# Kernel tuning notes

Hardware: AMD Instinct MI355X
Metric: run time of the kernel (lower is better)

Reference implementation:

```python
import jax, jax.numpy as jnp
import numpy as np

EPS = 1e-12


def _l2norm(x, axis):
    return x / jnp.maximum(jnp.linalg.norm(x, axis=axis, keepdims=True), EPS)


def _wn_weight(v, g):
    # weight norm over input axis (kernel_size=1): W = g * v / ||v||
    return g * v / jnp.maximum(jnp.linalg.norm(v, axis=0, keepdims=True), EPS)


def setup_inputs() -> dict:
    key = jax.random.key(0)
    ks = jax.random.split(key, 8)
    B, T, D = 16, 4096, 512
    N, K, d = 9, 1024, 8
    return {
        "z": jax.random.normal(ks[0], (B, T, D), dtype=jnp.float32),
        "in_v": jax.random.normal(ks[1], (N, D, d), dtype=jnp.float32) * 0.05,
        "in_g": jax.random.uniform(ks[2], (N, d), dtype=jnp.float32) + 0.5,
        "in_b": jax.random.normal(ks[3], (N, d), dtype=jnp.float32) * 0.01,
        "out_v": jax.random.normal(ks[4], (N, d, D), dtype=jnp.float32) * 0.05,
        "out_g": jax.random.uniform(ks[5], (N, D), dtype=jnp.float32) + 0.5,
        "out_b": jax.random.normal(ks[6], (N, D), dtype=jnp.float32) * 0.01,
        "codebooks": jax.random.normal(ks[7], (N, K, d), dtype=jnp.float32),
    }


def reference(z, in_v, in_g, in_b, out_v, out_g, out_b, codebooks):
    # Eval-mode ResidualVectorQuantize: n_quantizers = n_codebooks, mask all True.
    n_codebooks = codebooks.shape[0]
    residual = z
    z_q = jnp.zeros_like(z)
    commitment_loss = jnp.zeros((), z.dtype)
    codebook_loss = jnp.zeros((), z.dtype)
    codes, latents = [], []
    for i in range(n_codebooks):
        # in_proj (weight-normalized 1x1 conv == linear): [B,T,D] -> [B,T,d]
        W_in = _wn_weight(in_v[i], in_g[i])
        z_e = jnp.einsum("btd,dc->btc", residual, W_in) + in_b[i]
        # decode_latents: l2-normalize, pairwise sq-dist, nearest neighbor
        cb = codebooks[i]                      # [K, d] raw codebook
        enc_n = _l2norm(z_e, axis=-1)          # [B, T, d]
        cb_n = _l2norm(cb, axis=-1)            # [K, d]
        dist = (jnp.sum(enc_n * enc_n, -1, keepdims=True)
                - 2.0 * jnp.einsum("btc,kc->btk", enc_n, cb_n)
                + jnp.sum(cb_n * cb_n, -1))    # [B, T, K]
        indices = jnp.argmax(-dist, axis=-1)   # [B, T]
        z_q_i = cb[indices]                    # gather from raw codebook [B,T,d]
        # per-batch losses (mean over T, d)
        commit_i = jnp.mean((z_e - jax.lax.stop_gradient(z_q_i)) ** 2, axis=(1, 2))
        cbloss_i = jnp.mean((z_q_i - jax.lax.stop_gradient(z_e)) ** 2, axis=(1, 2))
        # straight-through estimator
        z_q_st = z_e + jax.lax.stop_gradient(z_q_i - z_e)
        # out_proj: [B,T,d] -> [B,T,D]
        W_out = _wn_weight(out_v[i], out_g[i])
        z_q_proj = jnp.einsum("btc,cd->btd", z_q_st, W_out) + out_b[i]
        z_q = z_q + z_q_proj
        residual = residual - z_q_proj
        commitment_loss = commitment_loss + commit_i.mean()
        codebook_loss = codebook_loss + cbloss_i.mean()
        codes.append(indices)
        latents.append(z_e)
    codes = jnp.stack(codes, axis=2)           # [B, T, N]
    latents = jnp.concatenate(latents, axis=2) # [B, T, N*d]
    return z_q, codes, latents, commitment_loss, codebook_loss
```

## Files before the change

kernel.cpp:

```cpp
#include <hip/hip_runtime.h>
#include <math.h>

#define ROWS   65536

#define WS_WPAD 0
#define WS_WOUT 49152
#define WS_CBT  86016
#define WS_SC   159744
#define WS_M    168960
#define WS_CACC 174144
#define WS_SOB  174216
#define WS_LOSS 174728

#define OUT_CODES 33554432
#define OUT_LAT   34144256
#define OUT_CLOSS 38862848
#define OUT_CBLOSS 38862849

__device__ __forceinline__ int pcol(int cc){ return (cc/9)*12 + (cc%9); }

__global__ __launch_bounds__(256) void prep1(const float* __restrict__ in_v,
    const float* __restrict__ in_g, const float* __restrict__ out_v,
    const float* __restrict__ out_g, const float* __restrict__ out_b,
    const float* __restrict__ cb, float* __restrict__ ws)
{
    int t = blockIdx.x*256 + threadIdx.x;
    if (t < 9216) {
        int i = t >> 10, k = t & 1023;
        const float* p = cb + (i*1024 + k)*8;
        float v[8]; float ssq = 0.f;
        #pragma unroll
        for (int c=0;c<8;c++){ v[c]=p[c]; ssq = fmaf(v[c],v[c],ssq); }
        float den = fmaxf(sqrtf(ssq), 1e-12f);
        float sc = 0.f;
        #pragma unroll
        for (int c=0;c<8;c++){ float cn = v[c]/den; ws[WS_CBT + (i*8+c)*1024 + k] = cn; sc = fmaf(cn,cn,sc); }
        ws[WS_SC + i*1024 + k] = sc;
    } else if (t < 13824) {
        int r = t - 9216; int j = r >> 9, tt = r & 511;
        float v[8]; float ssq = 0.f;
        #pragma unroll
        for (int a=0;a<8;a++){ v[a]=out_v[(j*8+a)*512+tt]; ssq=fmaf(v[a],v[a],ssq); }
        float den = fmaxf(sqrtf(ssq), 1e-12f);
        float g = out_g[j*512+tt];
        #pragma unroll
        for (int a=0;a<8;a++) ws[WS_WOUT + (j*8+a)*512 + tt] = g*v[a]/den;
    } else if (t < 18432) {
        int r = t - 13824;
        int w = r >> 6, l = r & 63;
        int i = w >> 3, c = w & 7;
        float v[8]; float ssq = 0.f;
        #pragma unroll
        for (int u=0;u<8;u++){ v[u] = in_v[(i*512 + l*8+u)*8 + c]; ssq = fmaf(v[u],v[u],ssq); }
        #pragma unroll
        for (int off=1; off<64; off<<=1) ssq += __shfl_xor(ssq, off, 64);
        float den = fmaxf(sqrtf(ssq), 1e-12f);
        float g = in_g[i*8+c];
        int pc = pcol(i*8+c);
        #pragma unroll
        for (int u=0;u<8;u++) ws[WS_WPAD + (l*8+u)*96 + pc] = g*v[u]/den;
    } else if (t < 18944) {
        int tt = t - 18432;
        float s = 0.f;
        for (int j=0;j<9;j++) s += out_b[j*512+tt];
        ws[WS_SOB + tt] = s;
    } else if (t == 18944) {
        *(double*)&ws[WS_LOSS] = 0.0;
    }
}

__global__ __launch_bounds__(256) void prep2(const float* __restrict__ out_b,
                                             float* __restrict__ ws)
{
    int g = blockIdx.x*256 + threadIdx.x;
    if (g < 41472) {
        int oi = g >> 3, part = g & 7;
        int j = oi / 576; int rem = oi % 576; int i = rem >> 6; int ab = rem & 63;
        int a = ab >> 3, b = ab & 7;
        int pc = pcol(i*8+b);
        const float* wo = ws + WS_WOUT + (j*8+a)*512 + part*64;
        const float* wp = ws + WS_WPAD + (part*64)*96 + pc;
        float s = 0.f;
        #pragma unroll
        for (int u=0; u<16; u++) {
            float4 w4 = *(const float4*)(wo + u*4);
            s = fmaf(w4.x, wp[(u*4+0)*96], s);
            s = fmaf(w4.y, wp[(u*4+1)*96], s);
            s = fmaf(w4.z, wp[(u*4+2)*96], s);
            s = fmaf(w4.w, wp[(u*4+3)*96], s);
        }
        #pragma unroll
        for (int off=1; off<8; off<<=1) s += __shfl_xor(s, off, 64);
        if (part == 0) ws[WS_M + oi] = s;
    } else if (g < 42048) {
        int r = g - 41472;
        int oi = r >> 3, part = r & 7;
        int i = oi >> 3, b = oi & 7;
        int pc = pcol(i*8+b);
        float s = 0.f;
        for (int u=0; u<64; u++) {
            int tt = part*64 + u;
            float bb = 0.f;
            for (int j=0;j<i;j++) bb += out_b[j*512+tt];
            s = fmaf(bb, ws[WS_WPAD + tt*96+pc], s);
        }
        #pragma unroll
        for (int off=1; off<8; off<<=1) s += __shfl_xor(s, off, 64);
        if (part == 0) ws[WS_CACC + oi] = s;
    }
}

__global__ __launch_bounds__(256) void gemm_in(const float* __restrict__ z,
    const float* __restrict__ in_b, const float* __restrict__ ws, float* __restrict__ out)
{
    __shared__ float AsT[32*132];
    __shared__ float Bs[32*96];
    int tid = threadIdx.x;
    int rowbase = blockIdx.x * 128;
    int tr = tid & 31, tc = tid >> 5;
    float acc[4][9];
    #pragma unroll
    for (int r=0;r<4;r++){
        #pragma unroll
        for(int c=0;c<9;c++) acc[r][c]=0.f;
    }
    int kq = tid & 7, rr = tid >> 3;
    for (int kk=0; kk<16; kk++) {
        #pragma unroll
        for (int p=0;p<4;p++){
            int row = rr + p*32;
            float4 a = *(const float4*)(z + (size_t)(rowbase+row)*512 + kk*32 + kq*4);
            AsT[(kq*4+0)*132 + row] = a.x;
            AsT[(kq*4+1)*132 + row] = a.y;
            AsT[(kq*4+2)*132 + row] = a.z;
            AsT[(kq*4+3)*132 + row] = a.w;
        }
        #pragma unroll
        for (int p=0;p<3;p++){
            int idx = p*256 + tid;
            *(float4*)(Bs + idx*4) = *(const float4*)(ws + WS_WPAD + kk*32*96 + idx*4);
        }
        __syncthreads();
        #pragma unroll 4
        for (int k=0;k<32;k++){
            float4 a  = *(const float4*)(AsT + k*132 + tr*4);
            float4 b0 = *(const float4*)(Bs + k*96 + tc*12);
            float4 b1 = *(const float4*)(Bs + k*96 + tc*12 + 4);
            float  b8 = Bs[k*96 + tc*12 + 8];
            float av[4] = {a.x,a.y,a.z,a.w};
            float bv[9] = {b0.x,b0.y,b0.z,b0.w,b1.x,b1.y,b1.z,b1.w,b8};
            #pragma unroll
            for (int r=0;r<4;r++){
                #pragma unroll
                for (int c=0;c<9;c++) acc[r][c] = fmaf(av[r], bv[c], acc[r][c]);
            }
        }
        __syncthreads();
    }
    #pragma unroll
    for (int c=0;c<9;c++){
        int cc = tc*9+c;
        float bias = in_b[cc];
        #pragma unroll
        for (int r=0;r<4;r++){
            int row = rowbase + tr*4 + r;
            out[OUT_LAT + (size_t)row*72 + cc] = acc[r][c] + bias;
        }
    }
}

__global__ __launch_bounds__(512, 4) void step_all(
    const float* __restrict__ cbooks, float* __restrict__ ws, float* __restrict__ out)
{
    __shared__ float lds_cb[8*1056];
    __shared__ float lds_sc[8*132];
    __shared__ float codes_lds[128*13];
    __shared__ float warr[8];

    int tid = threadIdx.x;
    int oct = tid & 7;
    int rowslot = tid >> 3;
    int rowbase = blockIdx.x * 128;
    const int kbase = oct*128;
    const float* cbo = lds_cb + oct*132;
    const float* sco = lds_sc + oct*132;

    float lacc = 0.f;

    for (int i=0; i<9; i++){
        __syncthreads();
        #pragma unroll
        for (int p=0;p<4;p++){
            int s = (p*512 + tid)*4;
            int c = s >> 10; int k = s & 1023; int o = k >> 7; int kk = k & 127;
            float4 v = *(const float4*)(ws + WS_CBT + i*8192 + s);
            *(float4*)(lds_cb + c*1056 + o*132 + kk) = v;
        }
        if (tid < 256){
            int s = tid*4;
            int o = s >> 7; int kk = s & 127;
            float4 v = *(const float4*)(ws + WS_SC + i*1024 + s);
            v.x *= 0.5f; v.y *= 0.5f; v.z *= 0.5f; v.w *= 0.5f;
            *(float4*)(lds_sc + o*132 + kk) = v;
        }
        __syncthreads();

        float zen[2][8];
        #pragma unroll
        for (int r=0;r<2;r++){
            int rib = r*64 + rowslot;
            int row = rowbase + rib;
            float* lat = out + OUT_LAT + (size_t)row*72 + i*8;
            float4 p0 = *(const float4*)(lat);
            float4 p1 = *(const float4*)(lat+4);
            float ze[8] = {p0.x,p0.y,p0.z,p0.w,p1.x,p1.y,p1.z,p1.w};
            #pragma unroll
            for (int b=0;b<8;b++) ze[b] -= ws[WS_CACC + i*8 + b];
            for (int j=0;j<i;j++){
                int kj = (int)codes_lds[rib*13 + j];
                const float* qp = cbooks + (size_t)(j*1024+kj)*8;
                float4 q0 = *(const float4*)(qp);
                float4 q1 = *(const float4*)(qp+4);
                float qa[8] = {q0.x,q0.y,q0.z,q0.w,q1.x,q1.y,q1.z,q1.w};
                const float* M = ws + WS_M + (j*9+i)*64;
                #pragma unroll
                for (int a=0;a<8;a++){
                    #pragma unroll
                    for (int b=0;b<8;b++) ze[b] = fmaf(-qa[a], M[a*8+b], ze[b]);
                }
            }
            float ssq = 0.f;
            #pragma unroll
            for (int c=0;c<8;c++) ssq = fmaf(ze[c],ze[c],ssq);
            float den = fmaxf(sqrtf(ssq), 1e-12f);
            float rden = 1.0f/den;
            if (oct == 0){
                float4 z0 = {ze[0],ze[1],ze[2],ze[3]};
                float4 z1 = {ze[4],ze[5],ze[6],ze[7]};
                *(float4*)(lat)   = z0;
                *(float4*)(lat+4) = z1;
            }
            #pragma unroll
            for (int c=0;c<8;c++) zen[r][c] = ze[c]*rden;
        }

        float bv[2]; int bk[2];
        #pragma unroll
        for (int r=0;r<2;r++){ bv[r] = -3.0e38f; bk[r] = kbase; }
        #pragma unroll 2
        for (int kk=0; kk<128; kk+=4){
            float4 v[8];
            #pragma unroll
            for (int c=0;c<8;c++) v[c] = *(const float4*)(cbo + c*1056 + kk);
            float4 hs = *(const float4*)(sco + kk);
            #pragma unroll
            for (int r=0;r<2;r++){
                float d0=-hs.x, d1=-hs.y, d2=-hs.z, d3=-hs.w;
                #pragma unroll
                for (int c=0;c<8;c++){
                    d0 = fmaf(zen[r][c], v[c].x, d0);
                    d1 = fmaf(zen[r][c], v[c].y, d1);
                    d2 = fmaf(zen[r][c], v[c].z, d2);
                    d3 = fmaf(zen[r][c], v[c].w, d3);
                }
                bool c0 = d0 > bv[r]; bk[r] = c0?(kbase+kk+0):bk[r]; bv[r] = c0?d0:bv[r];
                bool c1 = d1 > bv[r]; bk[r] = c1?(kbase+kk+1):bk[r]; bv[r] = c1?d1:bv[r];
                bool c2 = d2 > bv[r]; bk[r] = c2?(kbase+kk+2):bk[r]; bv[r] = c2?d2:bv[r];
                bool c3 = d3 > bv[r]; bk[r] = c3?(kbase+kk+3):bk[r]; bv[r] = c3?d3:bv[r];
            }
        }

        #pragma unroll
        for (int off=1; off<8; off<<=1){
            #pragma unroll
            for (int r=0;r<2;r++){
                float ov = __shfl_xor(bv[r], off, 64);
                int   ok = __shfl_xor(bk[r], off, 64);
                bool rep = (ov > bv[r]) || (ov == bv[r] && ok < bk[r]);
                bv[r] = rep ? ov : bv[r];
                bk[r] = rep ? ok : bk[r];
            }
        }
        if (oct == 0){
            #pragma unroll
            for (int r=0;r<2;r++){
                int rib = r*64 + rowslot;
                int row = rowbase + rib;
                out[OUT_CODES + (size_t)row*9 + i] = (float)bk[r];
                codes_lds[rib*13 + i] = (float)bk[r];
                const float* lat = out + OUT_LAT + (size_t)row*72 + i*8;
                const float* qp = cbooks + (size_t)(i*1024+bk[r])*8;
                float4 z0 = *(const float4*)(lat);
                float4 z1 = *(const float4*)(lat+4);
                float4 q0 = *(const float4*)(qp);
                float4 q1 = *(const float4*)(qp+4);
                float e0 = z0.x-q0.x, e1 = z0.y-q0.y, e2 = z0.z-q0.z, e3 = z0.w-q0.w;
                float e4 = z1.x-q1.x, e5 = z1.y-q1.y, e6 = z1.z-q1.z, e7 = z1.w-q1.w;
                lacc = fmaf(e0,e0,lacc); lacc = fmaf(e1,e1,lacc);
                lacc = fmaf(e2,e2,lacc); lacc = fmaf(e3,e3,lacc);
                lacc = fmaf(e4,e4,lacc); lacc = fmaf(e5,e5,lacc);
                lacc = fmaf(e6,e6,lacc); lacc = fmaf(e7,e7,lacc);
            }
        }
    }

    #pragma unroll
    for (int off=1; off<64; off<<=1) lacc += __shfl_xor(lacc, off, 64);
    if ((tid & 63)==0) warr[tid>>6] = lacc;
    __syncthreads();
    if (tid==0){
        double bs = 0.0;
        #pragma unroll
        for (int w=0; w<8; w++) bs += (double)warr[w];
        atomicAdd((double*)&ws[WS_LOSS], bs);
    }
}

__global__ __launch_bounds__(256) void gemm_out(const float* __restrict__ cbooks,
    const float* __restrict__ ws, float* __restrict__ out)
{
    __shared__ float QLT[72*140];
    __shared__ float Ws[72*140];
    int tid = threadIdx.x;
    int rowbase = blockIdx.x*128;
    if (tid < 128){
        int row = rowbase + tid;
        int rsw = tid + (tid>>5)*4;
        for (int j=0;j<9;j++){
            int kj = (int)out[OUT_CODES + (size_t)row*9 + j];
            const float* qp = cbooks + (size_t)(j*1024+kj)*8;
            float4 q0 = *(const float4*)qp;
            float4 q1 = *(const float4*)(qp+4);
            QLT[(j*8+0)*140 + rsw] = q0.x;
            QLT[(j*8+1)*140 + rsw] = q0.y;
            QLT[(j*8+2)*140 + rsw] = q0.z;
            QLT[(j*8+3)*140 + rsw] = q0.w;
            QLT[(j*8+4)*140 + rsw] = q1.x;
            QLT[(j*8+5)*140 + rsw] = q1.y;
            QLT[(j*8+6)*140 + rsw] = q1.z;
            QLT[(j*8+7)*140 + rsw] = q1.w;
        }
    }
    int tc = tid & 15, tr = tid >> 4;
    int aoff = tr*8 + (tr>>2)*4;
    int boff = tc*8 + (tc>>2)*4;
    for (int cc=0; cc<4; cc++){
        __syncthreads();
        #pragma unroll
        for (int p=0;p<9;p++){
            int idx = p*256 + tid;
            int jr = idx >> 5; int cq = idx & 31;
            float4 w = *(const float4*)(ws + WS_WOUT + jr*512 + cc*128 + cq*4);
            *(float4*)(Ws + jr*140 + cq*4 + (cq>>3)*4) = w;
        }
        __syncthreads();
        float acc[8][8];
        #pragma unroll
        for (int r=0;r<8;r++){
            #pragma unroll
            for (int c=0;c<8;c++) acc[r][c]=0.f;
        }
        #pragma unroll 2
        for (int k=0;k<72;k++){
            float4 a0 = *(const float4*)(QLT + k*140 + aoff);
            float4 a1 = *(const float4*)(QLT + k*140 + aoff + 4);
            float4 b0 = *(const float4*)(Ws + k*140 + boff);
            float4 b1 = *(const float4*)(Ws + k*140 + boff + 4);
            float av[8] = {a0.x,a0.y,a0.z,a0.w,a1.x,a1.y,a1.z,a1.w};
            float bw[8] = {b0.x,b0.y,b0.z,b0.w,b1.x,b1.y,b1.z,b1.w};
            #pragma unroll
            for (int r=0;r<8;r++){
                #pragma unroll
                for (int c=0;c<8;c++) acc[r][c] = fmaf(av[r], bw[c], acc[r][c]);
            }
        }
        float4 s0 = *(const float4*)(ws + WS_SOB + cc*128 + tc*8);
        float4 s1 = *(const float4*)(ws + WS_SOB + cc*128 + tc*8 + 4);
        #pragma unroll
        for (int r=0;r<8;r++){
            int row = rowbase + tr*8 + r;
            float4 o0 = {acc[r][0]+s0.x, acc[r][1]+s0.y, acc[r][2]+s0.z, acc[r][3]+s0.w};
            float4 o1 = {acc[r][4]+s1.x, acc[r][5]+s1.y, acc[r][6]+s1.z, acc[r][7]+s1.w};
            *(float4*)(out + (size_t)row*512 + cc*128 + tc*8)     = o0;
            *(float4*)(out + (size_t)row*512 + cc*128 + tc*8 + 4) = o1;
        }
    }
    if (blockIdx.x==0 && tid==0){
        double L = *(const double*)(ws + WS_LOSS);
        float lv = (float)(L * (1.0/524288.0));
        out[OUT_CLOSS]  = lv;
        out[OUT_CBLOSS] = lv;
    }
}

extern "C" void kernel_launch(void* const* d_in, const int* in_sizes, int n_in,
                              void* d_out, int out_size, void* d_ws, size_t ws_size,
                              hipStream_t stream) {
    const float* z     = (const float*)d_in[0];
    const float* in_v  = (const float*)d_in[1];
    const float* in_g  = (const float*)d_in[2];
    const float* in_b  = (const float*)d_in[3];
    const float* out_v = (const float*)d_in[4];
    const float* out_g = (const float*)d_in[5];
    const float* out_b = (const float*)d_in[6];
    const float* cb    = (const float*)d_in[7];
    float* out = (float*)d_out;
    float* ws  = (float*)d_ws;

    prep1<<<75, 256, 0, stream>>>(in_v, in_g, out_v, out_g, out_b, cb, ws);
    prep2<<<165, 256, 0, stream>>>(out_b, ws);
    gemm_in<<<512, 256, 0, stream>>>(z, in_b, ws, out);
    step_all<<<512, 512, 0, stream>>>(cb, ws, out);
    gemm_out<<<512, 256, 0, stream>>>(cb, ws, out);
}
```

Measured before the change: 677.2 us.

## Hold codebook slice in registers and reduce argmax across full wavefront

Restructures the nearest-codebook search so each lane keeps 16 codebook entries in registers and sweeps all 32 rows of its wave, with normalized latents shared via LDS. Removes the per-step LDS codebook staging and block-wide barriers, and shrinks blocks to 256 threads. In exchange each row needs a full 64-lane shuffle max plus ballot, and register pressure rises sharply, which may lower occupancy.

```diff
diff --git a/kernel.cpp b/kernel.cpp
--- a/kernel.cpp
+++ b/kernel.cpp
@@ -169,138 +169,126 @@
     }
 }
 
-__global__ __launch_bounds__(512, 4) void step_all(
+__global__ __launch_bounds__(256, 2) void step_all(
     const float* __restrict__ cbooks, float* __restrict__ ws, float* __restrict__ out)
 {
-    __shared__ float lds_cb[8*1056];
-    __shared__ float lds_sc[8*132];
+    __shared__ __align__(16) float zen_lds[4*32*12];
     __shared__ float codes_lds[128*13];
-    __shared__ float warr[8];
+    __shared__ float warr[4];
 
     int tid = threadIdx.x;
-    int oct = tid & 7;
-    int rowslot = tid >> 3;
-    int rowbase = blockIdx.x * 128;
-    const int kbase = oct*128;
-    const float* cbo = lds_cb + oct*132;
-    const float* sco = lds_sc + oct*132;
+    int w  = tid >> 6;
+    int l  = tid & 63;
+    int rowhalf = l >> 1;
+    int ah = l & 1;
+    int rowbase = blockIdx.x*128 + w*32;
+    int kb = l*16;
+    float* zen_w = zen_lds + w*384;
 
     float lacc = 0.f;
 
+    float4 cbr[4][8];
+    float4 hs4[4];
+
+    #pragma unroll 1
     for (int i=0; i<9; i++){
-        __syncthreads();
-        #pragma unroll
-        for (int p=0;p<4;p++){
-            int s = (p*512 + tid)*4;
-            int c = s >> 10; int k = s & 1023; int o = k >> 7; int kk = k & 127;
-            float4 v = *(const float4*)(ws + WS_CBT + i*8192 + s);
-            *(float4*)(lds_cb + c*1056 + o*132 + kk) = v;
-        }
-        if (tid < 256){
-            int s = tid*4;
-            int o = s >> 7; int kk = s & 127;
-            float4 v = *(const float4*)(ws + WS_SC + i*1024 + s);
-            v.x *= 0.5f; v.y *= 0.5f; v.z *= 0.5f; v.w *= 0.5f;
-            *(float4*)(lds_sc + o*132 + kk) = v;
-        }
-        __syncthreads();
-
-        float zen[2][8];
-        #pragma unroll
-        for (int r=0;r<2;r++){
-            int rib = r*64 + rowslot;
-            int row = rowbase + rib;
-            float* lat = out + OUT_LAT + (size_t)row*72 + i*8;
-            float4 p0 = *(const float4*)(lat);
-            float4 p1 = *(const float4*)(lat+4);
-            float ze[8] = {p0.x,p0.y,p0.z,p0.w,p1.x,p1.y,p1.z,p1.w};
-            #pragma unroll
-            for (int b=0;b<8;b++) ze[b] -= ws[WS_CACC + i*8 + b];
-            for (int j=0;j<i;j++){
-                int kj = (int)codes_lds[rib*13 + j];
-                const float* qp = cbooks + (size_t)(j*1024+kj)*8;
-                float4 q0 = *(const float4*)(qp);
-                float4 q1 = *(const float4*)(qp+4);
-                float qa[8] = {q0.x,q0.y,q0.z,q0.w,q1.x,q1.y,q1.z,q1.w};
-                const float* M = ws + WS_M + (j*9+i)*64;
+        #pragma unroll
+        for (int q=0;q<4;q++){
+            #pragma unroll
+            for (int c=0;c<8;c++)
+                cbr[q][c] = *(const float4*)(ws + WS_CBT + i*8192 + c*1024 + kb + q*4);
+            float4 s = *(const float4*)(ws + WS_SC + i*1024 + kb + q*4);
+            hs4[q].x = s.x * -0.5f; hs4[q].y = s.y * -0.5f;
+            hs4[q].z = s.z * -0.5f; hs4[q].w = s.w * -0.5f;
+        }
+
+        int row = rowbase + rowhalf;
+        int rib = w*32 + rowhalf;
+        float* lat = out + OUT_LAT + (size_t)row*72 + i*8;
+        float4 p0 = *(const float4*)(lat);
+        float4 p1 = *(const float4*)(lat+4);
+        float ze[8] = {p0.x,p0.y,p0.z,p0.w,p1.x,p1.y,p1.z,p1.w};
+        #pragma unroll
+        for (int b=0;b<8;b++) ze[b] -= ws[WS_CACC + i*8 + b];
+        #pragma unroll 1
+        for (int j=0;j<i;j++){
+            int kj = (int)codes_lds[rib*13 + j];
+            const float* qp = cbooks + (size_t)(j*1024+kj)*8;
+            float4 q0 = *(const float4*)(qp);
+            float4 q1 = *(const float4*)(qp+4);
+            float qa[8] = {q0.x,q0.y,q0.z,q0.w,q1.x,q1.y,q1.z,q1.w};
+            const float* M = ws + WS_M + (j*9+i)*64;
+            #pragma unroll
+            for (int a=0;a<8;a++){
                 #pragma unroll
-                for (int a=0;a<8;a++){
-                    #pragma unroll
-                    for (int b=0;b<8;b++) ze[b] = fmaf(-qa[a], M[a*8+b], ze[b]);
-                }
+                for (int b=0;b<8;b++) ze[b] = fmaf(-qa[a], M[a*8+b], ze[b]);
             }
-            float ssq = 0.f;
-            #pragma unroll
-            for (int c=0;c<8;c++) ssq = fmaf(ze[c],ze[c],ssq);
-            float den = fmaxf(sqrtf(ssq), 1e-12f);
-            float rden = 1.0f/den;
-            if (oct == 0){
-                float4 z0 = {ze[0],ze[1],ze[2],ze[3]};
-                float4 z1 = {ze[4],ze[5],ze[6],ze[7]};
-                *(float4*)(lat)   = z0;
-                *(float4*)(lat+4) = z1;
-            }
-            #pragma unroll
-            for (int c=0;c<8;c++) zen[r][c] = ze[c]*rden;
-        }
-
-        float bv[2]; int bk[2];
-        #pragma unroll
-        for (int r=0;r<2;r++){ bv[r] = -3.0e38f; bk[r] = kbase; }
+        }
+        float ssq = 0.f;
+        #pragma unroll
+        for (int c=0;c<8;c++) ssq = fmaf(ze[c],ze[c],ssq);
+        float den = fmaxf(sqrtf(ssq), 1e-12f);
+        float rden = 1.0f/den;
+        float zen[8];
+        #pragma unroll
+        for (int c=0;c<8;c++) zen[c] = ze[c]*rden;
+        if (ah == 0){
+            float4 n0 = {zen[0],zen[1],zen[2],zen[3]};
+            float4 n1 = {zen[4],zen[5],zen[6],zen[7]};
+            *(float4*)(zen_w + rowhalf*12)     = n0;
+            *(float4*)(zen_w + rowhalf*12 + 4) = n1;
+        } else {
+            float4 z0 = {ze[0],ze[1],ze[2],ze[3]};
+            float4 z1 = {ze[4],ze[5],ze[6],ze[7]};
+            *(float4*)(lat)   = z0;
+            *(float4*)(lat+4) = z1;
+        }
+
+        int ksave = 0;
         #pragma unroll 2
-        for (int kk=0; kk<128; kk+=4){
-            float4 v[8];
-            #pragma unroll
-            for (int c=0;c<8;c++) v[c] = *(const float4*)(cbo + c*1056 + kk);
-            float4 hs = *(const float4*)(sco + kk);
-            #pragma unroll
-            for (int r=0;r<2;r++){
-                float d0=-hs.x, d1=-hs.y, d2=-hs.z, d3=-hs.w;
+        for (int rr=0; rr<32; rr++){
+            float4 zv0 = *(const float4*)(zen_w + rr*12);
+            float4 zv1 = *(const float4*)(zen_w + rr*12 + 4);
+            float z[8] = {zv0.x,zv0.y,zv0.z,zv0.w,zv1.x,zv1.y,zv1.z,zv1.w};
+            float bv = -3.0e38f; int rel = 0;
+            #pragma unroll
+            for (int q=0;q<4;q++){
+                float d0 = hs4[q].x, d1 = hs4[q].y, d2 = hs4[q].z, d3 = hs4[q].w;
                 #pragma unroll
                 for (int c=0;c<8;c++){
-                    d0 = fmaf(zen[r][c], v[c].x, d0);
-                    d1 = fmaf(zen[r][c], v[c].y, d1);
-                    d2 = fmaf(zen[r][c], v[c].z, d2);
-                    d3 = fmaf(zen[r][c], v[c].w, d3);
+                    d0 = fmaf(z[c], cbr[q][c].x, d0);
+                    d1 = fmaf(z[c], cbr[q][c].y, d1);
+                    d2 = fmaf(z[c], cbr[q][c].z, d2);
+                    d3 = fmaf(z[c], cbr[q][c].w, d3);
                 }
-                bool c0 = d0 > bv[r]; bk[r] = c0?(kbase+kk+0):bk[r]; bv[r] = c0?d0:bv[r];
-                bool c1 = d1 > bv[r]; bk[r] = c1?(kbase+kk+1):bk[r]; bv[r] = c1?d1:bv[r];
-                bool c2 = d2 > bv[r]; bk[r] = c2?(kbase+kk+2):bk[r]; bv[r] = c2?d2:bv[r];
-                bool c3 = d3 > bv[r]; bk[r] = c3?(kbase+kk+3):bk[r]; bv[r] = c3?d3:bv[r];
+                bool c0 = d0 > bv; rel = c0 ? (q*4+0) : rel; bv = c0 ? d0 : bv;
+                bool c1 = d1 > bv; rel = c1 ? (q*4+1) : rel; bv = c1 ? d1 : bv;
+                bool c2 = d2 > bv; rel = c2 ? (q*4+2) : rel; bv = c2 ? d2 : bv;
+                bool c3 = d3 > bv; rel = c3 ? (q*4+3) : rel; bv = c3 ? d3 : bv;
             }
-        }
-
-        #pragma unroll
-        for (int off=1; off<8; off<<=1){
-            #pragma unroll
-            for (int r=0;r<2;r++){
-                float ov = __shfl_xor(bv[r], off, 64);
-                int   ok = __shfl_xor(bk[r], off, 64);
-                bool rep = (ov > bv[r]) || (ov == bv[r] && ok < bk[r]);
-                bv[r] = rep ? ov : bv[r];
-                bk[r] = rep ? ok : bk[r];
-            }
-        }
-        if (oct == 0){
-            #pragma unroll
-            for (int r=0;r<2;r++){
-                int rib = r*64 + rowslot;
-                int row = rowbase + rib;
-                out[OUT_CODES + (size_t)row*9 + i] = (float)bk[r];
-                codes_lds[rib*13 + i] = (float)bk[r];
-                const float* lat = out + OUT_LAT + (size_t)row*72 + i*8;
-                const float* qp = cbooks + (size_t)(i*1024+bk[r])*8;
-                float4 z0 = *(const float4*)(lat);
-                float4 z1 = *(const float4*)(lat+4);
-                float4 q0 = *(const float4*)(qp);
-                float4 q1 = *(const float4*)(qp+4);
-                float e0 = z0.x-q0.x, e1 = z0.y-q0.y, e2 = z0.z-q0.z, e3 = z0.w-q0.w;
-                float e4 = z1.x-q1.x, e5 = z1.y-q1.y, e6 = z1.z-q1.z, e7 = z1.w-q1.w;
-                lacc = fmaf(e0,e0,lacc); lacc = fmaf(e1,e1,lacc);
-                lacc = fmaf(e2,e2,lacc); lacc = fmaf(e3,e3,lacc);
-                lacc = fmaf(e4,e4,lacc); lacc = fmaf(e5,e5,lacc);
-                lacc = fmaf(e6,e6,lacc); lacc = fmaf(e7,e7,lacc);
-            }
+            int kfull = kb + rel;
+            float wm = bv;
+            #pragma unroll
+            for (int off=1; off<64; off<<=1) wm = fmaxf(wm, __shfl_xor(wm, off, 64));
+            unsigned long long msk = __ballot(bv == wm);
+            int ln = __ffsll((long long)msk) - 1;
+            int kwin = __shfl(kfull, ln, 64);
+            ksave = (rowhalf == rr) ? kwin : ksave;
+        }
+
+        if (ah == 0){
+            const float* qp = cbooks + (size_t)(i*1024+ksave)*8;
+            float4 q0 = *(const float4*)(qp);
+            float4 q1 = *(const float4*)(qp+4);
+            float e0 = ze[0]-q0.x, e1 = ze[1]-q0.y, e2 = ze[2]-q0.z, e3 = ze[3]-q0.w;
+            float e4 = ze[4]-q1.x, e5 = ze[5]-q1.y, e6 = ze[6]-q1.z, e7 = ze[7]-q1.w;
+            lacc = fmaf(e0,e0,lacc); lacc = fmaf(e1,e1,lacc);
+            lacc = fmaf(e2,e2,lacc); lacc = fmaf(e3,e3,lacc);
+            lacc = fmaf(e4,e4,lacc); lacc = fmaf(e5,e5,lacc);
+            lacc = fmaf(e6,e6,lacc); lacc = fmaf(e7,e7,lacc);
+        } else {
+            out[OUT_CODES + (size_t)row*9 + i] = (float)ksave;
+            codes_lds[rib*13 + i] = (float)ksave;
         }
     }
 
@@ -309,9 +297,7 @@
     if ((tid & 63)==0) warr[tid>>6] = lacc;
     __syncthreads();
     if (tid==0){
-        double bs = 0.0;
-        #pragma unroll
-        for (int w=0; w<8; w++) bs += (double)warr[w];
+        double bs = (double)warr[0]+(double)warr[1]+(double)warr[2]+(double)warr[3];
         atomicAdd((double*)&ws[WS_LOSS], bs);
     }
 }
@@ -350,8 +336,8 @@
         for (int p=0;p<9;p++){
             int idx = p*256 + tid;
             int jr = idx >> 5; int cq = idx & 31;
-            float4 w = *(const float4*)(ws + WS_WOUT + jr*512 + cc*128 + cq*4);
-            *(float4*)(Ws + jr*140 + cq*4 + (cq>>3)*4) = w;
+            float4 wv = *(const float4*)(ws + WS_WOUT + jr*512 + cc*128 + cq*4);
+            *(float4*)(Ws + jr*140 + cq*4 + (cq>>3)*4) = wv;
         }
         __syncthreads();
         float acc[8][8];
@@ -410,6 +396,6 @@
     prep1<<<75, 256, 0, stream>>>(in_v, in_g, out_v, out_g, out_b, cb, ws);
     prep2<<<165, 256, 0, stream>>>(out_b, ws);
     gemm_in<<<512, 256, 0, stream>>>(z, in_b, ws, out);
-    step_all<<<512, 512, 0, stream>>>(cb, ws, out);
+    step_all<<<512, 256, 0, stream>>>(cb, ws, out);
     gemm_out<<<512, 256, 0, stream>>>(cb, ws, out);
 }
```

New measurement: 598.7 us. 1.13x faster.
